# Optimization experiments

Hardware: AMD Instinct MI355X
Metric: run time of the kernel (lower is better)

Reference implementation:

```python
import jax, jax.numpy as jnp
import numpy as np

HID = 3072
HEADS = 24
HD = HID // HEADS  # 128
MLP = 4 * HID      # 12288
B, L, TXT = 1, 2304, 256
EPS_LN = 1e-6
EPS_RMS = 1e-6


def setup_inputs() -> dict:
    key = jax.random.key(0)
    ks = jax.random.split(key, 12)
    s = 0.02
    return {
        "hidden_states": jax.random.normal(ks[0], (B, L, HID), jnp.float32),
        "temb": jax.random.normal(ks[1], (B, HID), jnp.float32),
        "cos": jax.random.normal(ks[2], (L - TXT, HD), jnp.float32),
        "sin": jax.random.normal(ks[3], (L - TXT, HD), jnp.float32),
        "ada_w": jax.random.normal(ks[4], (HID, 3 * HID), jnp.float32) * s,
        "ada_b": jnp.zeros((3 * HID,), jnp.float32),
        "lin1_w": jax.random.normal(ks[5], (HID, 3 * HID + MLP), jnp.float32) * s,
        "lin1_b": jnp.zeros((3 * HID + MLP,), jnp.float32),
        "lin2_w": jax.random.normal(ks[6], (HID + MLP, HID), jnp.float32) * s,
        "lin2_b": jnp.zeros((HID,), jnp.float32),
        "qn_w": jnp.ones((HD,), jnp.float32),
        "kn_w": jnp.ones((HD,), jnp.float32),
        "txt_len": TXT,
    }


def _rotate_half(x):
    # interleaved pairs: (x0,x1) -> (-x1, x0)
    xr = x[..., 0::2]
    xi = x[..., 1::2]
    return jnp.stack([-xi, xr], axis=-1).reshape(x.shape)


def _rms_norm(x, w):
    var = jnp.mean(jnp.square(x), axis=-1, keepdims=True)
    return x * jax.lax.rsqrt(var + EPS_RMS) * w


def reference(hidden_states, temb, cos, sin, ada_w, ada_b, lin1_w, lin1_b,
              lin2_w, lin2_b, qn_w, kn_w, txt_len):
    # AdaLayerNormZeroSingle
    emb = jax.nn.silu(temb) @ ada_w + ada_b               # [B, 3*HID]
    shift, scale, gate = jnp.split(emb, 3, axis=-1)
    mu = jnp.mean(hidden_states, axis=-1, keepdims=True)
    var = jnp.var(hidden_states, axis=-1, keepdims=True)
    ln = (hidden_states - mu) * jax.lax.rsqrt(var + EPS_LN)
    norm_x = ln * (1.0 + scale[:, None, :]) + shift[:, None, :]

    # fused qkv + mlp-in projection
    proj = norm_x @ lin1_w + lin1_b                       # [B, L, 3*HID+MLP]
    qkv, mlp = proj[..., : 3 * HID], proj[..., 3 * HID:]
    qkv = qkv.reshape(B, L, 3, HEADS, HD)
    q, k, v = qkv[:, :, 0], qkv[:, :, 1], qkv[:, :, 2]    # [B, L, H, D]

    q = _rms_norm(q, qn_w)
    k = _rms_norm(k, kn_w)

    # RoPE on image tokens only (first L - txt_len)
    img = L - txt_len
    c = cos[None, :, None, :]
    s = sin[None, :, None, :]
    q_img = q[:, :img] * c + _rotate_half(q[:, :img]) * s
    k_img = k[:, :img] * c + _rotate_half(k[:, :img]) * s
    q = jnp.concatenate([q_img, q[:, img:]], axis=1)
    k = jnp.concatenate([k_img, k[:, img:]], axis=1)

    # SDPA (full, non-causal)
    scale_a = 1.0 / jnp.sqrt(jnp.asarray(HD, q.dtype))
    scores = jnp.einsum("blhd,bmhd->bhlm", q, k) * scale_a
    probs = jax.nn.softmax(scores, axis=-1)
    attn = jnp.einsum("bhlm,bmhd->blhd", probs, v).reshape(B, L, HID)

    # gated parallel-MLP output
    out = jnp.concatenate([attn, jax.nn.gelu(mlp, approximate=True)], axis=-1)
    out = out @ lin2_w + lin2_b
    return hidden_states + out * gate[:, None, :]
```

## Files before the change

### kernel.cpp

```cpp
#include <hip/hip_runtime.h>
#include <stdint.h>

#define HID   3072
#define LSEQ  2304
#define NH    24
#define HD    128
#define N1    21504
#define QKVW  9216
#define X2W   15360

typedef __bf16 bf16x8 __attribute__((ext_vector_type(8)));
typedef unsigned short u16x8 __attribute__((ext_vector_type(8)));
typedef float f32x4 __attribute__((ext_vector_type(4)));

#define MFMA(a,b,c) __builtin_amdgcn_mfma_f32_16x16x32_bf16((a),(b),(c),0,0,0)

#define GLOAD_LDS16(g, l) __builtin_amdgcn_global_load_lds( \
    (const __attribute__((address_space(1))) unsigned int*)(g), \
    (__attribute__((address_space(3))) unsigned int*)(l), 16, 0, 0)

__device__ __forceinline__ unsigned short f2b(float f){
  unsigned int u = __builtin_bit_cast(unsigned int, f);
  u += 0x7fffu + ((u >> 16) & 1u);
  return (unsigned short)(u >> 16);
}
__device__ __forceinline__ float b2f(unsigned short b){
  return __builtin_bit_cast(float, ((unsigned int)b) << 16);
}
__device__ __forceinline__ unsigned int pk2(float lo, float hi){
  return (unsigned int)f2b(lo) | ((unsigned int)f2b(hi) << 16);
}

__global__ void silu_k(const float* __restrict__ temb, float* __restrict__ st){
  int i = blockIdx.x*256 + threadIdx.x;
  if (i < HID){ float x = temb[i]; st[i] = x / (1.f + __expf(-x)); }
}

__global__ __launch_bounds__(256) void ada_k(const float* __restrict__ st,
                                             const float* __restrict__ aw,
                                             const float* __restrict__ ab,
                                             float* __restrict__ emb){
  int c = threadIdx.x & 31, g = threadIdx.x >> 5;
  int col = blockIdx.x*32 + c;
  float acc = 0.f;
  for (int k = g; k < HID; k += 8)
    acc += st[k] * aw[(size_t)k*QKVW + col];
  __shared__ float part[256];
  part[threadIdx.x] = acc;
  __syncthreads();
  if (threadIdx.x < 32){
    float s = 0.f;
    #pragma unroll
    for (int j = 0; j < 8; ++j) s += part[j*32 + threadIdx.x];
    int cc = blockIdx.x*32 + threadIdx.x;
    emb[cc] = s + ab[cc];
  }
}

__global__ __launch_bounds__(256) void ln_k(const float* __restrict__ hs,
                                            const float* __restrict__ emb,
                                            unsigned short* __restrict__ nx){
  int l = blockIdx.x, t = threadIdx.x;
  const float* row = hs + (size_t)l*HID;
  float x[12], s = 0.f, ss = 0.f;
  #pragma unroll
  for (int i = 0; i < 12; ++i){ x[i] = row[t + i*256]; s += x[i]; ss += x[i]*x[i]; }
  #pragma unroll
  for (int off = 32; off; off >>= 1){ s += __shfl_xor(s, off); ss += __shfl_xor(ss, off); }
  __shared__ float red[8];
  int w = t >> 6, lane = t & 63;
  if (!lane){ red[w] = s; red[4+w] = ss; }
  __syncthreads();
  s = red[0]+red[1]+red[2]+red[3];
  ss = red[4]+red[5]+red[6]+red[7];
  float mu = s * (1.f/HID);
  float var = ss * (1.f/HID) - mu*mu;
  float rstd = rsqrtf(var + 1e-6f);
  #pragma unroll
  for (int i = 0; i < 12; ++i){
    int c = t + i*256;
    float v = (x[i]-mu)*rstd*(1.f + emb[HID + c]) + emb[c];
    nx[(size_t)l*HID + c] = f2b(v);
  }
}

__global__ __launch_bounds__(256) void tconv_k(const float* __restrict__ W,
                                               unsigned short* __restrict__ WT,
                                               int ldw, int K){
  __shared__ unsigned short Ls[64*66];
  int k0 = blockIdx.x*64, n0 = blockIdx.y*64;
  int t = threadIdx.x;
  #pragma unroll
  for (int p = 0; p < 4; ++p){
    int idx = p*256 + t, row = idx >> 4, c4 = idx & 15;
    float4 f = *(const float4*)(W + (size_t)(k0+row)*ldw + n0 + c4*4);
    *(unsigned int*)&Ls[row*66 + c4*4]     = pk2(f.x, f.y);
    *(unsigned int*)&Ls[row*66 + c4*4 + 2] = pk2(f.z, f.w);
  }
  __syncthreads();
  #pragma unroll
  for (int p = 0; p < 2; ++p){
    int idx = p*256 + t, n = idx >> 3, ch = idx & 7;
    u16x8 r;
    #pragma unroll
    for (int j = 0; j < 8; ++j) r[j] = Ls[(ch*8 + j)*66 + n];
    *(uint4*)(WT + (size_t)(n0+n)*K + k0 + ch*8) = __builtin_bit_cast(uint4, r);
  }
}

template<int EPI>
__global__ __launch_bounds__(512, 2)
void gemm256_k(const unsigned short* __restrict__ A, const unsigned short* __restrict__ BT,
               const float* __restrict__ bias, int K, int NT,
               unsigned short* __restrict__ o16)
{
  __shared__ __align__(16) unsigned short As[4][256*32];
  __shared__ __align__(16) unsigned short Bs[4][256*32];
  const int t = threadIdx.x;
  const int m0 = blockIdx.y * 256, n0 = blockIdx.x * 256;
  const int w = t >> 6, lane = t & 63, quad = lane >> 4, l16 = lane & 15;
  const int wr = w >> 2, wc = w & 3;

  const unsigned short* aSrc[2];
  const unsigned short* bSrc[2];
  #pragma unroll
  for (int p = 0; p < 2; ++p){
    int lin = p*512 + t;
    int row = lin >> 2;
    int ch  = (lin & 3) ^ ((row >> 1) & 3);
    aSrc[p] = A  + (size_t)(m0 + row)*K + ch*8;
    bSrc[p] = BT + (size_t)(n0 + row)*K + ch*8;
  }
  const int ldsOff0 = w*512;
  const int ldsOff1 = 4096 + w*512;

#define STAGE_A(slot, pf) do{ \
    GLOAD_LDS16(aSrc[0] + (size_t)(pf)*32, &As[slot][ldsOff0]); \
    GLOAD_LDS16(aSrc[1] + (size_t)(pf)*32, &As[slot][ldsOff1]); }while(0)
#define STAGE_B(slot, pf) do{ \
    GLOAD_LDS16(bSrc[0] + (size_t)(pf)*32, &Bs[slot][ldsOff0]); \
    GLOAD_LDS16(bSrc[1] + (size_t)(pf)*32, &Bs[slot][ldsOff1]); }while(0)

  const int kSwz  = (quad ^ ((l16 >> 1) & 3)) * 8;
  const int aBase = (wr*128 + l16)*32 + kSwz;
  const int bBase = (wc*64  + l16)*32 + kSwz;

  f32x4 acc[8][4];
  #pragma unroll
  for (int i = 0; i < 8; ++i)
    #pragma unroll
    for (int j = 0; j < 4; ++j) acc[i][j] = (f32x4){0.f,0.f,0.f,0.f};

  STAGE_A(0, 0); STAGE_B(0, 0);
  STAGE_A(1, 1); STAGE_B(1, 1);
  STAGE_A(2, 2); STAGE_B(2, 2);
  asm volatile("s_waitcnt vmcnt(8)" ::: "memory");
  __builtin_amdgcn_sched_barrier(0);
  __builtin_amdgcn_s_barrier();

  for (int kt = 0; kt < NT; ++kt){
    const int slot  = kt & 3;
    const int wslot = (kt + 3) & 3;
    const int pf    = (kt + 3 < NT) ? (kt + 3) : (NT - 1);
    bf16x8 af[4], bf[4];

    STAGE_A(wslot, pf);
    #pragma unroll
    for (int i = 0; i < 4; ++i)
      af[i] = __builtin_bit_cast(bf16x8, *(const uint4*)&As[slot][aBase + i*512]);
    #pragma unroll
    for (int i = 0; i < 4; ++i)
      bf[i] = __builtin_bit_cast(bf16x8, *(const uint4*)&Bs[slot][bBase + i*512]);
    __builtin_amdgcn_s_barrier();
    asm volatile("s_waitcnt lgkmcnt(0)" ::: "memory");
    __builtin_amdgcn_sched_barrier(0);
    __builtin_amdgcn_s_setprio(1);
    #pragma unroll
    for (int mi = 0; mi < 4; ++mi)
      #pragma unroll
      for (int ni = 0; ni < 4; ++ni)
        acc[mi][ni] = MFMA(af[mi], bf[ni], acc[mi][ni]);
    __builtin_amdgcn_s_setprio(0);

    STAGE_B(wslot, pf);
    #pragma unroll
    for (int i = 0; i < 4; ++i)
      af[i] = __builtin_bit_cast(bf16x8, *(const uint4*)&As[slot][aBase + 2048 + i*512]);
    __builtin_amdgcn_s_barrier();
    asm volatile("s_waitcnt lgkmcnt(0)" ::: "memory");
    __builtin_amdgcn_sched_barrier(0);
    __builtin_amdgcn_s_setprio(1);
    #pragma unroll
    for (int mi = 0; mi < 4; ++mi)
      #pragma unroll
      for (int ni = 0; ni < 4; ++ni)
        acc[4+mi][ni] = MFMA(af[mi], bf[ni], acc[4+mi][ni]);
    __builtin_amdgcn_s_setprio(0);
    asm volatile("s_waitcnt vmcnt(8)" ::: "memory");
    __builtin_amdgcn_sched_barrier(0);
    __builtin_amdgcn_s_barrier();
  }
#undef STAGE_A
#undef STAGE_B

  asm volatile("s_waitcnt vmcnt(0)" ::: "memory");

  #pragma unroll
  for (int mi = 0; mi < 8; ++mi){
    #pragma unroll
    for (int ni = 0; ni < 4; ++ni){
      const int gn = n0 + wc*64 + ni*16 + l16;
      const float bs = bias[gn];
      #pragma unroll
      for (int r = 0; r < 4; ++r){
        const int gm = m0 + wr*128 + mi*16 + quad*4 + r;
        float v = acc[mi][ni][r] + bs;
        if (EPI == 1){
          o16[(size_t)gm*QKVW + gn] = f2b(v);
        } else {
          float e = __expf(1.5957691216057308f*(v + 0.044715f*v*v*v));
          float th = 1.f - 2.f/(e + 1.f);
          o16[(size_t)gm*X2W + HID + gn] = f2b(0.5f*v*(1.f + th));
        }
      }
    }
  }
}

__global__ __launch_bounds__(512, 2)
void gemm256n_k(const unsigned short* __restrict__ A, const unsigned short* __restrict__ BT,
                const float* __restrict__ bias, int K, int NT,
                float* __restrict__ of, const float* __restrict__ hid,
                const float* __restrict__ emb)
{
  __shared__ __align__(16) unsigned short As[4][128*32];
  __shared__ __align__(16) unsigned short Bs[4][256*32];
  const int t = threadIdx.x;
  const int m0 = blockIdx.y * 128, n0 = blockIdx.x * 256;
  const int w = t >> 6, lane = t & 63, quad = lane >> 4, l16 = lane & 15;
  const int wr = w >> 2, wc = w & 3;

  const unsigned short* aSrc;
  { int row = t >> 2, ch = (t & 3) ^ ((row >> 1) & 3);
    aSrc = A + (size_t)(m0 + row)*K + ch*8; }
  const unsigned short* bSrc[2];
  #pragma unroll
  for (int p = 0; p < 2; ++p){
    int lin = p*512 + t, row = lin >> 2, ch = (lin & 3) ^ ((row >> 1) & 3);
    bSrc[p] = BT + (size_t)(n0 + row)*K + ch*8;
  }
  const int aOff  = w*512;
  const int bOff0 = w*512, bOff1 = 4096 + w*512;

#define STAGE(slot, pf) do{ \
    GLOAD_LDS16(aSrc    + (size_t)(pf)*32, &As[slot][aOff]); \
    GLOAD_LDS16(bSrc[0] + (size_t)(pf)*32, &Bs[slot][bOff0]); \
    GLOAD_LDS16(bSrc[1] + (size_t)(pf)*32, &Bs[slot][bOff1]); }while(0)

  const int kSwz  = (quad ^ ((l16 >> 1) & 3)) * 8;
  const int aBase = (wr*64 + l16)*32 + kSwz;
  const int bBase = (wc*64 + l16)*32 + kSwz;

  f32x4 acc[4][4];
  #pragma unroll
  for (int i = 0; i < 4; ++i)
    #pragma unroll
    for (int j = 0; j < 4; ++j) acc[i][j] = (f32x4){0.f,0.f,0.f,0.f};

  STAGE(0, 0); STAGE(1, 1); STAGE(2, 2);
  asm volatile("s_waitcnt vmcnt(6)" ::: "memory");
  __builtin_amdgcn_sched_barrier(0);
  __builtin_amdgcn_s_barrier();

  for (int kt = 0; kt < NT; ++kt){
    const int slot  = kt & 3;
    const int wslot = (kt + 3) & 3;
    const int pf    = (kt + 3 < NT) ? (kt + 3) : (NT - 1);
    bf16x8 af[4], bf[4];

    STAGE(wslot, pf);
    #pragma unroll
    for (int i = 0; i < 4; ++i)
      af[i] = __builtin_bit_cast(bf16x8, *(const uint4*)&As[slot][aBase + i*512]);
    #pragma unroll
    for (int i = 0; i < 4; ++i)
      bf[i] = __builtin_bit_cast(bf16x8, *(const uint4*)&Bs[slot][bBase + i*512]);
    __builtin_amdgcn_s_barrier();
    asm volatile("s_waitcnt lgkmcnt(0)" ::: "memory");
    __builtin_amdgcn_sched_barrier(0);
    __builtin_amdgcn_s_setprio(1);
    #pragma unroll
    for (int mi = 0; mi < 4; ++mi)
      #pragma unroll
      for (int ni = 0; ni < 4; ++ni)
        acc[mi][ni] = MFMA(af[mi], bf[ni], acc[mi][ni]);
    __builtin_amdgcn_s_setprio(0);
    asm volatile("s_waitcnt vmcnt(6)" ::: "memory");
    __builtin_amdgcn_sched_barrier(0);
    __builtin_amdgcn_s_barrier();
  }
#undef STAGE

  asm volatile("s_waitcnt vmcnt(0)" ::: "memory");

  #pragma unroll
  for (int mi = 0; mi < 4; ++mi){
    #pragma unroll
    for (int ni = 0; ni < 4; ++ni){
      const int gn = n0 + wc*64 + ni*16 + l16;
      const float bs = bias[gn];
      #pragma unroll
      for (int r = 0; r < 4; ++r){
        const int gm = m0 + wr*64 + mi*16 + quad*4 + r;
        float v = acc[mi][ni][r] + bs;
        of[(size_t)gm*HID + gn] = hid[(size_t)gm*HID + gn] + v * emb[2*HID + gn];
      }
    }
  }
}

__global__ __launch_bounds__(256) void qknorm_k(unsigned short* __restrict__ qkv,
                                                const float* __restrict__ qn,
                                                const float* __restrict__ kn,
                                                const float* __restrict__ cosp,
                                                const float* __restrict__ sinp,
                                                const int* __restrict__ txtp){
  int img = LSEQ - txtp[0];
  int rid = blockIdx.x*4 + (threadIdx.x >> 6);
  int lane = threadIdx.x & 63;
  int which = rid / (NH*LSEQ);
  int rem   = rid % (NH*LSEQ);
  int h = rem / LSEQ, l = rem % LSEQ;
  unsigned short* p = qkv + (size_t)l*QKVW + which*HID + h*HD + lane*2;
  unsigned int both = *(const unsigned int*)p;
  float x0 = b2f((unsigned short)(both & 0xffffu));
  float x1 = b2f((unsigned short)(both >> 16));
  float ss = x0*x0 + x1*x1;
  #pragma unroll
  for (int off = 32; off; off >>= 1) ss += __shfl_xor(ss, off);
  float r = rsqrtf(ss*(1.f/HD) + 1e-6f);
  const float* wv = which ? kn : qn;
  float y0 = x0*r*wv[lane*2], y1 = x1*r*wv[lane*2+1];
  if (l < img){
    float c0 = cosp[l*HD + lane*2], c1 = cosp[l*HD + lane*2 + 1];
    float s0 = sinp[l*HD + lane*2], s1 = sinp[l*HD + lane*2 + 1];
    float t0 = y0*c0 - y1*s0;
    float t1 = y1*c1 + y0*s1;
    y0 = t0; y1 = t1;
  }
  if (which == 0){ y0 *= 0.08838834764831845f; y1 *= 0.08838834764831845f; }
  *(unsigned int*)p = pk2(y0, y1);
}

__global__ __launch_bounds__(256) void vtrans_k(const unsigned short* __restrict__ qkv,
                                                unsigned short* __restrict__ vT){
  __shared__ __align__(16) unsigned short Ls[64*136];
  int h = blockIdx.y, m0 = blockIdx.x*64, t = threadIdx.x;
  #pragma unroll
  for (int p = 0; p < 4; ++p){
    int lin = p*256 + t, m = lin >> 4, ch = lin & 15;
    *(uint4*)&Ls[m*136 + ch*8] =
      *(const uint4*)(qkv + (size_t)(m0+m)*QKVW + 2*HID + h*HD + ch*8);
  }
  __syncthreads();
  #pragma unroll
  for (int p = 0; p < 4; ++p){
    int lin = p*256 + t, d = lin >> 3, ch = lin & 7;
    u16x8 r;
    #pragma unroll
    for (int j = 0; j < 8; ++j) r[j] = Ls[(ch*8 + j)*136 + d];
    *(uint4*)(vT + (size_t)h*HD*LSEQ + (size_t)d*LSEQ + m0 + ch*8) =
      __builtin_bit_cast(uint4, r);
  }
}

__global__ __launch_bounds__(256)
void attn_k(const unsigned short* __restrict__ qkv,
            const unsigned short* __restrict__ vT,
            unsigned short* __restrict__ x2)
{
  __shared__ __align__(16) unsigned short Ks[32*136];
  __shared__ __align__(16) unsigned short Vt[128*40];
  __shared__ __align__(16) unsigned short Ps[4*16*40];
  const int h = blockIdx.y, qb = blockIdx.x*64;
  const int t = threadIdx.x, w = t >> 6, lane = t & 63, quad = lane >> 4, l16 = lane & 15;

  bf16x8 aq[4];
  {
    const unsigned short* qp = qkv + (size_t)(qb + w*16 + l16)*QKVW + h*HD;
    #pragma unroll
    for (int dt = 0; dt < 4; ++dt)
      aq[dt] = __builtin_bit_cast(bf16x8, *(const uint4*)(qp + dt*32 + quad*8));
  }
  f32x4 o[8];
  #pragma unroll
  for (int i = 0; i < 8; ++i) o[i] = (f32x4){0.f,0.f,0.f,0.f};
  float mr[4] = {-1e30f,-1e30f,-1e30f,-1e30f};
  float lr[4] = {0.f,0.f,0.f,0.f};

  const unsigned short* kb = qkv + HID + h*HD;
  const unsigned short* vb = vT + (size_t)h*HD*LSEQ;
  unsigned short* pw = &Ps[w*16*40];

  for (int m0 = 0; m0 < LSEQ; m0 += 32){
    __syncthreads();
    #pragma unroll
    for (int p = 0; p < 2; ++p){
      int lin = p*256 + t, kr = lin >> 4, ch = lin & 15;
      *(uint4*)&Ks[kr*136 + ch*8] = *(const uint4*)(kb + (size_t)(m0+kr)*QKVW + ch*8);
    }
    #pragma unroll
    for (int p = 0; p < 2; ++p){
      int lin = p*256 + t, d = lin >> 2, ch = lin & 3;
      *(uint4*)&Vt[d*40 + ch*8] = *(const uint4*)(vb + (size_t)d*LSEQ + m0 + ch*8);
    }
    __syncthreads();

    f32x4 s0 = (f32x4){0.f,0.f,0.f,0.f}, s1 = s0;
    __builtin_amdgcn_s_setprio(1);
    #pragma unroll
    for (int dt = 0; dt < 4; ++dt){
      bf16x8 k0 = __builtin_bit_cast(bf16x8, *(const uint4*)&Ks[l16*136 + dt*32 + quad*8]);
      bf16x8 k1 = __builtin_bit_cast(bf16x8, *(const uint4*)&Ks[(16+l16)*136 + dt*32 + quad*8]);
      s0 = MFMA(aq[dt], k0, s0);
      s1 = MFMA(aq[dt], k1, s1);
    }
    __builtin_amdgcn_s_setprio(0);
    #pragma unroll
    for (int r = 0; r < 4; ++r){
      float mx = fmaxf(s0[r], s1[r]);
      mx = fmaxf(mx, __shfl_xor(mx, 1));
      mx = fmaxf(mx, __shfl_xor(mx, 2));
      mx = fmaxf(mx, __shfl_xor(mx, 4));
      mx = fmaxf(mx, __shfl_xor(mx, 8));
      float mn = fmaxf(mr[r], mx);
      float al = __expf(mr[r] - mn);
      float p0 = __expf(s0[r] - mn), p1 = __expf(s1[r] - mn);
      float rs = p0 + p1;
      rs += __shfl_xor(rs, 1);
      rs += __shfl_xor(rs, 2);
      rs += __shfl_xor(rs, 4);
      rs += __shfl_xor(rs, 8);
      lr[r] = lr[r]*al + rs;
      mr[r] = mn;
      #pragma unroll
      for (int i = 0; i < 8; ++i) o[i][r] *= al;
      int q = quad*4 + r;
      pw[q*40 + l16]      = f2b(p0);
      pw[q*40 + 16 + l16] = f2b(p1);
    }
    bf16x8 pa = __builtin_bit_cast(bf16x8, *(const uint4*)&pw[l16*40 + quad*8]);
    __builtin_amdgcn_s_setprio(1);
    #pragma unroll
    for (int i = 0; i < 8; ++i){
      bf16x8 vv = __builtin_bit_cast(bf16x8, *(const uint4*)&Vt[(i*16 + l16)*40 + quad*8]);
      o[i] = MFMA(pa, vv, o[i]);
    }
    __builtin_amdgcn_s_setprio(0);
  }
  #pragma unroll
  for (int i = 0; i < 8; ++i){
    #pragma unroll
    for (int r = 0; r < 4; ++r){
      int q = qb + w*16 + quad*4 + r;
      x2[(size_t)q*X2W + h*HD + i*16 + l16] = f2b(o[i][r] / lr[r]);
    }
  }
}

extern "C" void kernel_launch(void* const* d_in, const int* in_sizes, int n_in,
                              void* d_out, int out_size, void* d_ws, size_t ws_size,
                              hipStream_t stream) {
  const float* hs     = (const float*)d_in[0];
  const float* temb   = (const float*)d_in[1];
  const float* cosp   = (const float*)d_in[2];
  const float* sinp   = (const float*)d_in[3];
  const float* ada_w  = (const float*)d_in[4];
  const float* ada_b  = (const float*)d_in[5];
  const float* lin1_w = (const float*)d_in[6];
  const float* lin1_b = (const float*)d_in[7];
  const float* lin2_w = (const float*)d_in[8];
  const float* lin2_b = (const float*)d_in[9];
  const float* qn     = (const float*)d_in[10];
  const float* kn     = (const float*)d_in[11];
  const int*   txt    = (const int*)d_in[12];
  float* out = (float*)d_out;

  char* ws = (char*)d_ws;
  float*          st  = (float*)ws;
  float*          emb = (float*)(ws + 12288);
  unsigned short* nx  = (unsigned short*)(ws + 49152);
  unsigned short* qkv = (unsigned short*)(ws + 14204928);
  unsigned short* x2  = (unsigned short*)(ws + 56672256);
  unsigned short* vT  = (unsigned short*)(ws + 127451136);
  unsigned short* wt  = (unsigned short*)(ws + 141606912);

  silu_k<<<12, 256, 0, stream>>>(temb, st);
  ada_k<<<288, 256, 0, stream>>>(st, ada_w, ada_b, emb);
  ln_k<<<LSEQ, 256, 0, stream>>>(hs, emb, nx);

  tconv_k<<<dim3(HID/64, QKVW/64), 256, 0, stream>>>(lin1_w, wt, N1, HID);
  gemm256_k<1><<<dim3(QKVW/256, LSEQ/256), 512, 0, stream>>>(nx, wt, lin1_b, HID, HID/32, qkv);
  tconv_k<<<dim3(HID/64, (N1-QKVW)/64), 256, 0, stream>>>(lin1_w + QKVW, wt, N1, HID);
  gemm256_k<3><<<dim3((N1-QKVW)/256, LSEQ/256), 512, 0, stream>>>(nx, wt, lin1_b + QKVW, HID, HID/32, x2);

  qknorm_k<<<(2*NH*LSEQ)/4, 256, 0, stream>>>(qkv, qn, kn, cosp, sinp, txt);
  vtrans_k<<<dim3(LSEQ/64, NH), 256, 0, stream>>>(qkv, vT);
  attn_k<<<dim3(LSEQ/64, NH), 256, 0, stream>>>(qkv, vT, x2);

  tconv_k<<<dim3(X2W/64, HID/64), 256, 0, stream>>>(lin2_w, wt, HID, X2W);
  gemm256n_k<<<dim3(HID/256, LSEQ/128), 512, 0, stream>>>(x2, wt, lin2_b, X2W, X2W/32,
                                                          out, hs, emb);
}
```

Baseline: 1.917 ms.

## Restructure GEMMs to BK=64 double-buffered pipeline and merge lin1 launches

Both GEMM kernels move from a 4-stage ring of K=32 tiles to a 2-stage double buffer of K=64 tiles with an 8-chunk XOR swizzle. The MFMA work is split into four interleaved phases so the global-to-LDS prefetch is issued during the last compute phase. The two lin1 GEMMs (qkv and MLP) and their weight conversions are merged into one launch, with the epilogue chosen per block by column range. The lin2 GEMM tile shape changes to 256x128, and the vT buffer now reuses the normalized-input workspace. The aim is fewer barriers per K element, fewer launches and better occupancy of the wave tail, at the risk of less prefetch depth to hide memory latency.

```diff
diff --git a/kernel.cpp b/kernel.cpp
--- a/kernel.cpp
+++ b/kernel.cpp
@@ -29,6 +29,9 @@
 }
 __device__ __forceinline__ unsigned int pk2(float lo, float hi){
   return (unsigned int)f2b(lo) | ((unsigned int)f2b(hi) << 16);
+}
+__device__ __forceinline__ bf16x8 ldsv(const unsigned short* p){
+  return __builtin_bit_cast(bf16x8, *(const uint4*)p);
 }
 
 __global__ void silu_k(const float* __restrict__ temb, float* __restrict__ st){
@@ -108,42 +111,39 @@
   }
 }
 
-template<int EPI>
 __global__ __launch_bounds__(512, 2)
-void gemm256_k(const unsigned short* __restrict__ A, const unsigned short* __restrict__ BT,
+void gemm8p1_k(const unsigned short* __restrict__ A, const unsigned short* __restrict__ BT,
                const float* __restrict__ bias, int K, int NT,
-               unsigned short* __restrict__ o16)
+               unsigned short* __restrict__ qo, unsigned short* __restrict__ xo)
 {
-  __shared__ __align__(16) unsigned short As[4][256*32];
-  __shared__ __align__(16) unsigned short Bs[4][256*32];
+  __shared__ __align__(16) unsigned short As[2][256*64];
+  __shared__ __align__(16) unsigned short Bs[2][256*64];
   const int t = threadIdx.x;
   const int m0 = blockIdx.y * 256, n0 = blockIdx.x * 256;
   const int w = t >> 6, lane = t & 63, quad = lane >> 4, l16 = lane & 15;
   const int wr = w >> 2, wc = w & 3;
 
-  const unsigned short* aSrc[2];
-  const unsigned short* bSrc[2];
-  #pragma unroll
-  for (int p = 0; p < 2; ++p){
-    int lin = p*512 + t;
-    int row = lin >> 2;
-    int ch  = (lin & 3) ^ ((row >> 1) & 3);
-    aSrc[p] = A  + (size_t)(m0 + row)*K + ch*8;
-    bSrc[p] = BT + (size_t)(n0 + row)*K + ch*8;
-  }
-  const int ldsOff0 = w*512;
-  const int ldsOff1 = 4096 + w*512;
-
-#define STAGE_A(slot, pf) do{ \
-    GLOAD_LDS16(aSrc[0] + (size_t)(pf)*32, &As[slot][ldsOff0]); \
-    GLOAD_LDS16(aSrc[1] + (size_t)(pf)*32, &As[slot][ldsOff1]); }while(0)
-#define STAGE_B(slot, pf) do{ \
-    GLOAD_LDS16(bSrc[0] + (size_t)(pf)*32, &Bs[slot][ldsOff0]); \
-    GLOAD_LDS16(bSrc[1] + (size_t)(pf)*32, &Bs[slot][ldsOff1]); }while(0)
-
-  const int kSwz  = (quad ^ ((l16 >> 1) & 3)) * 8;
-  const int aBase = (wr*128 + l16)*32 + kSwz;
-  const int bBase = (wc*64  + l16)*32 + kSwz;
+  const int r0  = t >> 3;
+  const int chs = (t & 7) ^ (r0 & 7);
+  const unsigned short* aS = A  + (size_t)(m0 + r0)*K + chs*8;
+  const unsigned short* bS = BT + (size_t)(n0 + r0)*K + chs*8;
+  const int dst = t*8;
+
+#define STG1(c, pf) do{ const size_t _k = (size_t)(pf)*64; \
+    GLOAD_LDS16(aS + _k,                 &As[c][dst]); \
+    GLOAD_LDS16(aS +  64*(size_t)K + _k, &As[c][4096  + dst]); \
+    GLOAD_LDS16(aS + 128*(size_t)K + _k, &As[c][8192  + dst]); \
+    GLOAD_LDS16(aS + 192*(size_t)K + _k, &As[c][12288 + dst]); \
+    GLOAD_LDS16(bS + _k,                 &Bs[c][dst]); \
+    GLOAD_LDS16(bS +  64*(size_t)K + _k, &Bs[c][4096  + dst]); \
+    GLOAD_LDS16(bS + 128*(size_t)K + _k, &Bs[c][8192  + dst]); \
+    GLOAD_LDS16(bS + 192*(size_t)K + _k, &Bs[c][12288 + dst]); }while(0)
+
+  const int sz = l16 & 7;
+  const int aR = (wr*128 + l16)*64;
+  const int bR = (wc*64  + l16)*64;
+  const int c0 = (quad ^ sz)*8;
+  const int c1 = ((4 + quad) ^ sz)*8;
 
   f32x4 acc[8][4];
   #pragma unroll
@@ -151,60 +151,97 @@
     #pragma unroll
     for (int j = 0; j < 4; ++j) acc[i][j] = (f32x4){0.f,0.f,0.f,0.f};
 
-  STAGE_A(0, 0); STAGE_B(0, 0);
-  STAGE_A(1, 1); STAGE_B(1, 1);
-  STAGE_A(2, 2); STAGE_B(2, 2);
+  STG1(0, 0); STG1(1, 1);
   asm volatile("s_waitcnt vmcnt(8)" ::: "memory");
   __builtin_amdgcn_sched_barrier(0);
   __builtin_amdgcn_s_barrier();
 
   for (int kt = 0; kt < NT; ++kt){
-    const int slot  = kt & 3;
-    const int wslot = (kt + 3) & 3;
-    const int pf    = (kt + 3 < NT) ? (kt + 3) : (NT - 1);
-    bf16x8 af[4], bf[4];
-
-    STAGE_A(wslot, pf);
-    #pragma unroll
-    for (int i = 0; i < 4; ++i)
-      af[i] = __builtin_bit_cast(bf16x8, *(const uint4*)&As[slot][aBase + i*512]);
-    #pragma unroll
-    for (int i = 0; i < 4; ++i)
-      bf[i] = __builtin_bit_cast(bf16x8, *(const uint4*)&Bs[slot][bBase + i*512]);
+    const int c  = kt & 1;
+    const int pf = (kt + 2 < NT) ? (kt + 2) : (NT - 1);
+    const unsigned short* Ac = As[c];
+    const unsigned short* Bc = Bs[c];
+    bf16x8 af0[4][2], af1[4][2], bf[2][2];
+
+    #pragma unroll
+    for (int mt = 0; mt < 4; ++mt){
+      af0[mt][0] = ldsv(Ac + aR + mt*1024 + c0);
+      af0[mt][1] = ldsv(Ac + aR + mt*1024 + c1);
+    }
+    #pragma unroll
+    for (int nt = 0; nt < 2; ++nt){
+      bf[nt][0] = ldsv(Bc + bR + nt*1024 + c0);
+      bf[nt][1] = ldsv(Bc + bR + nt*1024 + c1);
+    }
     __builtin_amdgcn_s_barrier();
     asm volatile("s_waitcnt lgkmcnt(0)" ::: "memory");
     __builtin_amdgcn_sched_barrier(0);
     __builtin_amdgcn_s_setprio(1);
     #pragma unroll
-    for (int mi = 0; mi < 4; ++mi)
-      #pragma unroll
-      for (int ni = 0; ni < 4; ++ni)
-        acc[mi][ni] = MFMA(af[mi], bf[ni], acc[mi][ni]);
-    __builtin_amdgcn_s_setprio(0);
-
-    STAGE_B(wslot, pf);
-    #pragma unroll
-    for (int i = 0; i < 4; ++i)
-      af[i] = __builtin_bit_cast(bf16x8, *(const uint4*)&As[slot][aBase + 2048 + i*512]);
+    for (int mt = 0; mt < 4; ++mt)
+      #pragma unroll
+      for (int nt = 0; nt < 2; ++nt){
+        acc[mt][nt] = MFMA(af0[mt][0], bf[nt][0], acc[mt][nt]);
+        acc[mt][nt] = MFMA(af0[mt][1], bf[nt][1], acc[mt][nt]);
+      }
+    __builtin_amdgcn_s_setprio(0);
+
+    #pragma unroll
+    for (int mt = 0; mt < 4; ++mt){
+      af1[mt][0] = ldsv(Ac + aR + 4096 + mt*1024 + c0);
+      af1[mt][1] = ldsv(Ac + aR + 4096 + mt*1024 + c1);
+    }
     __builtin_amdgcn_s_barrier();
     asm volatile("s_waitcnt lgkmcnt(0)" ::: "memory");
     __builtin_amdgcn_sched_barrier(0);
     __builtin_amdgcn_s_setprio(1);
     #pragma unroll
-    for (int mi = 0; mi < 4; ++mi)
-      #pragma unroll
-      for (int ni = 0; ni < 4; ++ni)
-        acc[4+mi][ni] = MFMA(af[mi], bf[ni], acc[4+mi][ni]);
+    for (int mt = 0; mt < 4; ++mt)
+      #pragma unroll
+      for (int nt = 0; nt < 2; ++nt){
+        acc[4+mt][nt] = MFMA(af1[mt][0], bf[nt][0], acc[4+mt][nt]);
+        acc[4+mt][nt] = MFMA(af1[mt][1], bf[nt][1], acc[4+mt][nt]);
+      }
+    __builtin_amdgcn_s_setprio(0);
+
+    #pragma unroll
+    for (int nt = 0; nt < 2; ++nt){
+      bf[nt][0] = ldsv(Bc + bR + 2048 + nt*1024 + c0);
+      bf[nt][1] = ldsv(Bc + bR + 2048 + nt*1024 + c1);
+    }
+    __builtin_amdgcn_s_barrier();
+    asm volatile("s_waitcnt lgkmcnt(0)" ::: "memory");
+    __builtin_amdgcn_sched_barrier(0);
+    __builtin_amdgcn_s_setprio(1);
+    #pragma unroll
+    for (int mt = 0; mt < 4; ++mt)
+      #pragma unroll
+      for (int nt = 0; nt < 2; ++nt){
+        acc[4+mt][2+nt] = MFMA(af1[mt][0], bf[nt][0], acc[4+mt][2+nt]);
+        acc[4+mt][2+nt] = MFMA(af1[mt][1], bf[nt][1], acc[4+mt][2+nt]);
+      }
+    __builtin_amdgcn_s_setprio(0);
+
+    __builtin_amdgcn_s_barrier();
+    STG1(c, pf);
+    __builtin_amdgcn_s_setprio(1);
+    #pragma unroll
+    for (int mt = 0; mt < 4; ++mt)
+      #pragma unroll
+      for (int nt = 0; nt < 2; ++nt){
+        acc[mt][2+nt] = MFMA(af0[mt][0], bf[nt][0], acc[mt][2+nt]);
+        acc[mt][2+nt] = MFMA(af0[mt][1], bf[nt][1], acc[mt][2+nt]);
+      }
     __builtin_amdgcn_s_setprio(0);
     asm volatile("s_waitcnt vmcnt(8)" ::: "memory");
     __builtin_amdgcn_sched_barrier(0);
     __builtin_amdgcn_s_barrier();
   }
-#undef STAGE_A
-#undef STAGE_B
+#undef STG1
 
   asm volatile("s_waitcnt vmcnt(0)" ::: "memory");
 
+  const bool isQ = (n0 < QKVW);
   #pragma unroll
   for (int mi = 0; mi < 8; ++mi){
     #pragma unroll
@@ -215,12 +252,12 @@
       for (int r = 0; r < 4; ++r){
         const int gm = m0 + wr*128 + mi*16 + quad*4 + r;
         float v = acc[mi][ni][r] + bs;
-        if (EPI == 1){
-          o16[(size_t)gm*QKVW + gn] = f2b(v);
+        if (isQ){
+          qo[(size_t)gm*QKVW + gn] = f2b(v);
         } else {
           float e = __expf(1.5957691216057308f*(v + 0.044715f*v*v*v));
           float th = 1.f - 2.f/(e + 1.f);
-          o16[(size_t)gm*X2W + HID + gn] = f2b(0.5f*v*(1.f + th));
+          xo[(size_t)gm*X2W + HID + (gn - QKVW)] = f2b(0.5f*v*(1.f + th));
         }
       }
     }
@@ -228,38 +265,36 @@
 }
 
 __global__ __launch_bounds__(512, 2)
-void gemm256n_k(const unsigned short* __restrict__ A, const unsigned short* __restrict__ BT,
-                const float* __restrict__ bias, int K, int NT,
-                float* __restrict__ of, const float* __restrict__ hid,
-                const float* __restrict__ emb)
+void gemm8p2_k(const unsigned short* __restrict__ A, const unsigned short* __restrict__ BT,
+               const float* __restrict__ bias, int K, int NT,
+               float* __restrict__ of, const float* __restrict__ hid,
+               const float* __restrict__ emb)
 {
-  __shared__ __align__(16) unsigned short As[4][128*32];
-  __shared__ __align__(16) unsigned short Bs[4][256*32];
+  __shared__ __align__(16) unsigned short As[2][256*64];
+  __shared__ __align__(16) unsigned short Bs[2][128*64];
   const int t = threadIdx.x;
-  const int m0 = blockIdx.y * 128, n0 = blockIdx.x * 256;
+  const int m0 = blockIdx.y * 256, n0 = blockIdx.x * 128;
   const int w = t >> 6, lane = t & 63, quad = lane >> 4, l16 = lane & 15;
-  const int wr = w >> 2, wc = w & 3;
-
-  const unsigned short* aSrc;
-  { int row = t >> 2, ch = (t & 3) ^ ((row >> 1) & 3);
-    aSrc = A + (size_t)(m0 + row)*K + ch*8; }
-  const unsigned short* bSrc[2];
-  #pragma unroll
-  for (int p = 0; p < 2; ++p){
-    int lin = p*512 + t, row = lin >> 2, ch = (lin & 3) ^ ((row >> 1) & 3);
-    bSrc[p] = BT + (size_t)(n0 + row)*K + ch*8;
-  }
-  const int aOff  = w*512;
-  const int bOff0 = w*512, bOff1 = 4096 + w*512;
-
-#define STAGE(slot, pf) do{ \
-    GLOAD_LDS16(aSrc    + (size_t)(pf)*32, &As[slot][aOff]); \
-    GLOAD_LDS16(bSrc[0] + (size_t)(pf)*32, &Bs[slot][bOff0]); \
-    GLOAD_LDS16(bSrc[1] + (size_t)(pf)*32, &Bs[slot][bOff1]); }while(0)
-
-  const int kSwz  = (quad ^ ((l16 >> 1) & 3)) * 8;
-  const int aBase = (wr*64 + l16)*32 + kSwz;
-  const int bBase = (wc*64 + l16)*32 + kSwz;
+  const int wr = w >> 1, wc = w & 1;
+
+  const int r0  = t >> 3;
+  const int chs = (t & 7) ^ (r0 & 7);
+  const unsigned short* aS = A  + (size_t)(m0 + r0)*K + chs*8;
+  const unsigned short* bS = BT + (size_t)(n0 + r0)*K + chs*8;
+  const int dst = t*8;
+
+#define STG2(c, pf) do{ const size_t _k = (size_t)(pf)*64; \
+    GLOAD_LDS16(aS + _k,                 &As[c][dst]); \
+    GLOAD_LDS16(aS +  64*(size_t)K + _k, &As[c][4096  + dst]); \
+    GLOAD_LDS16(aS + 128*(size_t)K + _k, &As[c][8192  + dst]); \
+    GLOAD_LDS16(aS + 192*(size_t)K + _k, &As[c][12288 + dst]); \
+    GLOAD_LDS16(bS + _k,                 &Bs[c][dst]); \
+    GLOAD_LDS16(bS +  64*(size_t)K + _k, &Bs[c][4096  + dst]); }while(0)
+
+  const int sz = l16 & 7;
+  const int aR = (wr*64 + l16)*64;
+  const int bR = (wc*64 + l16)*64;
+  const int c0 = (quad ^ sz)*8, c1 = ((4 + quad) ^ sz)*8;
 
   f32x4 acc[4][4];
   #pragma unroll
@@ -267,39 +302,75 @@
     #pragma unroll
     for (int j = 0; j < 4; ++j) acc[i][j] = (f32x4){0.f,0.f,0.f,0.f};
 
-  STAGE(0, 0); STAGE(1, 1); STAGE(2, 2);
+  STG2(0, 0); STG2(1, 1);
   asm volatile("s_waitcnt vmcnt(6)" ::: "memory");
   __builtin_amdgcn_sched_barrier(0);
   __builtin_amdgcn_s_barrier();
 
   for (int kt = 0; kt < NT; ++kt){
-    const int slot  = kt & 3;
-    const int wslot = (kt + 3) & 3;
-    const int pf    = (kt + 3 < NT) ? (kt + 3) : (NT - 1);
-    bf16x8 af[4], bf[4];
-
-    STAGE(wslot, pf);
-    #pragma unroll
-    for (int i = 0; i < 4; ++i)
-      af[i] = __builtin_bit_cast(bf16x8, *(const uint4*)&As[slot][aBase + i*512]);
-    #pragma unroll
-    for (int i = 0; i < 4; ++i)
-      bf[i] = __builtin_bit_cast(bf16x8, *(const uint4*)&Bs[slot][bBase + i*512]);
+    const int c  = kt & 1;
+    const int pf = (kt + 2 < NT) ? (kt + 2) : (NT - 1);
+    const unsigned short* Ac = As[c];
+    const unsigned short* Bc = Bs[c];
+    bf16x8 af[4][2], bf[2][2];
+
+    #pragma unroll
+    for (int mt = 0; mt < 4; ++mt){
+      af[mt][0] = ldsv(Ac + aR + mt*1024 + c0);
+      af[mt][1] = ldsv(Ac + aR + mt*1024 + c1);
+    }
+    #pragma unroll
+    for (int nt = 0; nt < 2; ++nt){
+      bf[nt][0] = ldsv(Bc + bR + nt*1024 + c0);
+      bf[nt][1] = ldsv(Bc + bR + nt*1024 + c1);
+    }
     __builtin_amdgcn_s_barrier();
     asm volatile("s_waitcnt lgkmcnt(0)" ::: "memory");
     __builtin_amdgcn_sched_barrier(0);
     __builtin_amdgcn_s_setprio(1);
     #pragma unroll
-    for (int mi = 0; mi < 4; ++mi)
-      #pragma unroll
-      for (int ni = 0; ni < 4; ++ni)
-        acc[mi][ni] = MFMA(af[mi], bf[ni], acc[mi][ni]);
+    for (int mt = 0; mt < 4; ++mt)
+      #pragma unroll
+      for (int nt = 0; nt < 2; ++nt){
+        acc[mt][nt] = MFMA(af[mt][0], bf[nt][0], acc[mt][nt]);
+        acc[mt][nt] = MFMA(af[mt][1], bf[nt][1], acc[mt][nt]);
+      }
+    __builtin_amdgcn_s_setprio(0);
+
+    #pragma unroll
+    for (int nt = 0; nt < 2; ++nt){
+      bf[nt][0] = ldsv(Bc + bR + 2048 + nt*1024 + c0);
+      bf[nt][1] = ldsv(Bc + bR + 2048 + nt*1024 + c1);
+    }
+    __builtin_amdgcn_s_barrier();
+    asm volatile("s_waitcnt lgkmcnt(0)" ::: "memory");
+    __builtin_amdgcn_sched_barrier(0);
+    __builtin_amdgcn_s_setprio(1);
+    #pragma unroll
+    for (int mt = 0; mt < 2; ++mt)
+      #pragma unroll
+      for (int nt = 0; nt < 2; ++nt){
+        acc[mt][2+nt] = MFMA(af[mt][0], bf[nt][0], acc[mt][2+nt]);
+        acc[mt][2+nt] = MFMA(af[mt][1], bf[nt][1], acc[mt][2+nt]);
+      }
+    __builtin_amdgcn_s_setprio(0);
+
+    __builtin_amdgcn_s_barrier();
+    STG2(c, pf);
+    __builtin_amdgcn_s_setprio(1);
+    #pragma unroll
+    for (int mt = 2; mt < 4; ++mt)
+      #pragma unroll
+      for (int nt = 0; nt < 2; ++nt){
+        acc[mt][2+nt] = MFMA(af[mt][0], bf[nt][0], acc[mt][2+nt]);
+        acc[mt][2+nt] = MFMA(af[mt][1], bf[nt][1], acc[mt][2+nt]);
+      }
     __builtin_amdgcn_s_setprio(0);
     asm volatile("s_waitcnt vmcnt(6)" ::: "memory");
     __builtin_amdgcn_sched_barrier(0);
     __builtin_amdgcn_s_barrier();
   }
-#undef STAGE
+#undef STG2
 
   asm volatile("s_waitcnt vmcnt(0)" ::: "memory");
 
@@ -309,11 +380,12 @@
     for (int ni = 0; ni < 4; ++ni){
       const int gn = n0 + wc*64 + ni*16 + l16;
       const float bs = bias[gn];
+      const float gt = emb[2*HID + gn];
       #pragma unroll
       for (int r = 0; r < 4; ++r){
         const int gm = m0 + wr*64 + mi*16 + quad*4 + r;
         float v = acc[mi][ni][r] + bs;
-        of[(size_t)gm*HID + gn] = hid[(size_t)gm*HID + gn] + v * emb[2*HID + gn];
+        of[(size_t)gm*HID + gn] = hid[(size_t)gm*HID + gn] + v * gt;
       }
     }
   }
@@ -490,25 +562,24 @@
   float*          st  = (float*)ws;
   float*          emb = (float*)(ws + 12288);
   unsigned short* nx  = (unsigned short*)(ws + 49152);
+  unsigned short* vT  = nx;
   unsigned short* qkv = (unsigned short*)(ws + 14204928);
   unsigned short* x2  = (unsigned short*)(ws + 56672256);
-  unsigned short* vT  = (unsigned short*)(ws + 127451136);
-  unsigned short* wt  = (unsigned short*)(ws + 141606912);
+  unsigned short* wt  = (unsigned short*)(ws + 127451136);
 
   silu_k<<<12, 256, 0, stream>>>(temb, st);
   ada_k<<<288, 256, 0, stream>>>(st, ada_w, ada_b, emb);
   ln_k<<<LSEQ, 256, 0, stream>>>(hs, emb, nx);
 
-  tconv_k<<<dim3(HID/64, QKVW/64), 256, 0, stream>>>(lin1_w, wt, N1, HID);
-  gemm256_k<1><<<dim3(QKVW/256, LSEQ/256), 512, 0, stream>>>(nx, wt, lin1_b, HID, HID/32, qkv);
-  tconv_k<<<dim3(HID/64, (N1-QKVW)/64), 256, 0, stream>>>(lin1_w + QKVW, wt, N1, HID);
-  gemm256_k<3><<<dim3((N1-QKVW)/256, LSEQ/256), 512, 0, stream>>>(nx, wt, lin1_b + QKVW, HID, HID/32, x2);
+  tconv_k<<<dim3(HID/64, N1/64), 256, 0, stream>>>(lin1_w, wt, N1, HID);
+  gemm8p1_k<<<dim3(N1/256, LSEQ/256), 512, 0, stream>>>(nx, wt, lin1_b, HID, HID/64,
+                                                        qkv, x2);
 
   qknorm_k<<<(2*NH*LSEQ)/4, 256, 0, stream>>>(qkv, qn, kn, cosp, sinp, txt);
   vtrans_k<<<dim3(LSEQ/64, NH), 256, 0, stream>>>(qkv, vT);
   attn_k<<<dim3(LSEQ/64, NH), 256, 0, stream>>>(qkv, vT, x2);
 
   tconv_k<<<dim3(X2W/64, HID/64), 256, 0, stream>>>(lin2_w, wt, HID, X2W);
-  gemm256n_k<<<dim3(HID/256, LSEQ/128), 512, 0, stream>>>(x2, wt, lin2_b, X2W, X2W/32,
-                                                          out, hs, emb);
-}
+  gemm8p2_k<<<dim3(HID/128, LSEQ/256), 512, 0, stream>>>(x2, wt, lin2_b, X2W, X2W/64,
+                                                         out, hs, emb);
+}
```

After: 1.807 ms. -5.8%, faster.
